# Kernel optimization log

Measured on AMD Instinct MI355X. Metric: run time of the kernel, lower is better.

The kernel has to match this reference:

```python
import jax, jax.numpy as jnp
import numpy as np

E = 8_388_608  # total edges across batched graphs
G = 4096       # num_graphs


def setup_inputs() -> dict:
    key = jax.random.key(0)
    k1, k2, k3 = jax.random.split(key, 3)
    edge_scores = jax.random.normal(k1, (E,), dtype=jnp.float32)
    # edge_batch: sorted segment ids in [0, G), as in PyG batched graphs
    edge_batch = jnp.sort(jax.random.randint(k2, (E,), 0, G)).astype(jnp.int32)
    candidate_mask = jax.random.bernoulli(k3, 0.5, (E,))
    return {
        "edge_scores": edge_scores,
        "edge_batch": edge_batch,
        "candidate_mask": candidate_mask,
        "num_graphs": G,
        "k": 32,
    }


def reference(edge_scores, edge_batch, candidate_mask, num_graphs, k):
    """Segmented top-k edge selection (GFlowNetActor._select_topk_candidate_edges).

    Faithful fixed-shape formulation: candidate edges come in as a boolean mask
    over all E edges (the rollout builds cand_edges = nonzero(candidate_mask)),
    and the kept top-k-per-graph edges go out as a boolean pruned mask (the
    rollout scatters the returned indices back into pruned_mask). Also returns
    the score values gated by the pruned mask (differentiable output).
    """
    n = edge_scores.shape[0]
    neg_inf = jnp.finfo(jnp.float32).min
    # Non-candidates get -inf so they sort to the back of each segment
    s = jnp.where(candidate_mask, edge_scores.astype(jnp.float32), neg_inf)
    # Sort by score descending, then stably by segment id -> within each
    # graph edges appear in descending-score order (same double-argsort as torch)
    order_score = jnp.argsort(-s, stable=True)
    order_seg = jnp.argsort(edge_batch[order_score], stable=True)
    perm = order_score[order_seg]          # [E] edge ids sorted by (seg asc, score desc)
    seg_sorted = edge_batch[perm]          # [E]
    # Segment starts via bincount + exclusive cumsum
    counts = jnp.bincount(seg_sorted, length=num_graphs)
    start = jnp.concatenate(
        [jnp.zeros(1, jnp.int32), jnp.cumsum(counts)[:-1].astype(jnp.int32)]
    )
    rank = jnp.arange(n, dtype=jnp.int32) - start[seg_sorted]
    keep_sorted = (rank < k) & candidate_mask[perm]
    # Scatter keep flags back to original edge order
    pruned_mask = jnp.zeros(n, dtype=bool).at[perm].set(keep_sorted)
    pruned_scores = jnp.where(pruned_mask, edge_scores, jnp.float32(0.0))
    return pruned_mask, pruned_scores
```

## Files before the change

### kernel.cpp

```cpp
#include <hip/hip_runtime.h>
#include <stdint.h>

#define G_NUM 4096
#define BLOCK 256
#define WPB   4
#define WCH   12
#define CAPW  (64 * 4 * WCH - 3)
#define HBW   1024
#define CLSW  128

typedef unsigned long long ull;

__device__ __forceinline__ void wsync() {
    asm volatile("s_waitcnt lgkmcnt(0)" ::: "memory");
}

__device__ __forceinline__ unsigned int order_bits(float f) {
    unsigned int b = __float_as_uint(f);
    return (b & 0x80000000u) ? ~b : (b | 0x80000000u);
}
__device__ __forceinline__ float inv_order_bits(unsigned int ob) {
    return __uint_as_float((ob & 0x80000000u) ? (ob & 0x7FFFFFFFu) : ~ob);
}
__device__ __forceinline__ int physb(int b) { return ((b & 15) << 6) | (b >> 4); }

__global__ void prep_kernel(const int* __restrict__ batch, int* __restrict__ start,
                            const unsigned int* __restrict__ mraw, int* __restrict__ flag,
                            int E) {
    if (blockIdx.x == 0 && threadIdx.x < 64) {
        int lane = threadIdx.x;
        bool allI = true, allF = true;
        for (int i = lane; i < 256; i += 64) {
            unsigned int w = mraw[i];
            if (w > 1u) allI = false;
            if (w != 0u && w != 0x3F800000u) allF = false;
        }
        allI = __all(allI);
        allF = __all(allF);
        if (lane == 0) *flag = (allI || allF) ? 0 : 2;
    }
    int t = blockIdx.x * blockDim.x + threadIdx.x;
    if (t > G_NUM) return;
    if (t == G_NUM) { start[G_NUM] = E; return; }
    int lo = 0, hi = E;
    while (lo < hi) {
        int mid = (lo + hi) >> 1;
        if (batch[mid] < t) lo = mid + 1; else hi = mid;
    }
    start[t] = lo;
}

template <int NPT>
__device__ __forceinline__ void wave_sel(unsigned int* hist, int lane, int kk,
                                         int& bsel, unsigned int& cgt,
                                         unsigned int& csel, unsigned int& mtot)
{
    unsigned int h[NPT];
    unsigned int S = 0u;
    const int b0 = lane * NPT;
    #pragma unroll
    for (int j = 0; j < NPT; ++j) {
        int pb = physb(b0 + j);
        h[j] = hist[pb]; S += h[j]; hist[pb] = 0u;
    }
    unsigned int v = S;
    #pragma unroll
    for (int off = 1; off < 64; off <<= 1) {
        unsigned int o = __shfl_down(v, off, 64);
        if (lane + off < 64) v += o;
    }
    mtot = __shfl(v, 0, 64);
    unsigned int run = v - S;
    int fj = -1; unsigned int fc = 0u, fs = 0u;
    #pragma unroll
    for (int j = NPT - 1; j >= 0; --j) {
        unsigned int inc = run + h[j];
        if (fj < 0 && (unsigned)kk <= inc && (unsigned)kk > run) { fj = j; fc = run; fs = h[j]; }
        run = inc;
    }
    ull bm = __ballot(fj >= 0);
    int wl = (int)(__ffsll((long long)bm) - 1);
    bsel = __shfl(b0 + fj, wl, 64);
    cgt  = __shfl(fc, wl, 64);
    csel = __shfl(fs, wl, 64);
}

__global__ __launch_bounds__(BLOCK, 4) void topk_kernel(
    const float* __restrict__ scores, const void* __restrict__ maskp,
    const int* __restrict__ start, const int* __restrict__ kp,
    const int* __restrict__ flagp, float* __restrict__ out_mask,
    float* __restrict__ out_scores, int E)
{
    __shared__ unsigned int hist_s[WPB][HBW];
    __shared__ ull          cls_s[WPB][CLSW];
    __shared__ unsigned int ccnt_s[WPB];

    const int tid  = threadIdx.x;
    const int lane = tid & 63;
    const int w    = tid >> 6;
    const int g    = blockIdx.x * WPB + w;

    const int s0 = start[g];
    const int s1 = start[g + 1];
    const int len = s1 - s0;
    if (len <= 0) return;

    const int k     = *kp;
    const int mflag = *flagp;
    unsigned int* hist = hist_s[w];
    ull*          cls  = cls_s[w];

    auto getmask = [&](int i) -> bool {
        if (mflag == 2) return ((const unsigned char*)maskp)[i] != 0;
        return ((const int*)maskp)[i] != 0;
    };

    if (k <= 0) {
        for (int i = s0 + lane; i < s1; i += 64) { out_mask[i] = 0.0f; out_scores[i] = 0.0f; }
        return;
    }

    if (len <= CAPW) {
        const int a0 = s0 & ~3;
        const int dl = a0 - s0;
        unsigned int key[4 * WCH];
        ull candm = 0ull;

        #pragma unroll
        for (int j = 0; j < HBW / 64; ++j) hist[physb(lane + 64 * j)] = 0u;
        if (lane == 0) ccnt_s[w] = 0u;

        #pragma unroll
        for (int q = 0; q < WCH; ++q) {
            const int g0 = a0 + 4 * (q * 64 + lane);
            unsigned int cm4 = 0u;
            if (g0 >= s0 && g0 + 4 <= s1) {
                float4 f = *(const float4*)(scores + g0);
                key[4*q+0] = order_bits(f.x); key[4*q+1] = order_bits(f.y);
                key[4*q+2] = order_bits(f.z); key[4*q+3] = order_bits(f.w);
                if (mflag == 2) {
                    unsigned int mw = *(const unsigned int*)((const unsigned char*)maskp + g0);
                    if (mw & 0x000000FFu) cm4 |= 1u;
                    if (mw & 0x0000FF00u) cm4 |= 2u;
                    if (mw & 0x00FF0000u) cm4 |= 4u;
                    if (mw & 0xFF000000u) cm4 |= 8u;
                } else {
                    int4 mw = *(const int4*)((const int*)maskp + g0);
                    if (mw.x) cm4 |= 1u; if (mw.y) cm4 |= 2u;
                    if (mw.z) cm4 |= 4u; if (mw.w) cm4 |= 8u;
                }
            } else if (g0 < s1 && g0 + 4 > s0) {
                #pragma unroll
                for (int j = 0; j < 4; ++j) {
                    int gi = g0 + j; key[4*q+j] = 0u;
                    if (gi >= s0 && gi < s1) {
                        key[4*q+j] = order_bits(scores[gi]);
                        if (getmask(gi)) cm4 |= 1u << j;
                    }
                }
            } else {
                #pragma unroll
                for (int j = 0; j < 4; ++j) key[4*q+j] = 0u;
            }
            candm |= (ull)cm4 << (4 * q);
        }
        wsync();

        #pragma unroll
        for (int v = 0; v < 4 * WCH; ++v)
            if ((candm >> v) & 1ull) atomicAdd(&hist[physb((int)(key[v] >> 22))], 1u);
        wsync();

        int bsel; unsigned int cgt, csel, m;
        wave_sel<HBW / 64>(hist, lane, k, bsel, cgt, csel, m);

        const bool keepall = (m <= (unsigned)k);
        unsigned int P = 0u;
        int licut = 0x7FFFFFFF;

        if (!keepall) {
            int kk2 = k - (int)cgt;

            if (csel <= CLSW) {
                #pragma unroll
                for (int v = 0; v < 4 * WCH; ++v) {
                    if (((candm >> v) & 1ull) && (int)(key[v] >> 22) == bsel) {
                        int q = v >> 2;
                        int li = dl + 4 * (q * 64 + lane) + (v & 3);
                        cls[atomicAdd(&ccnt_s[w], 1u)] = ((ull)key[v] << 32) | (unsigned)li;
                    }
                }
                wsync();
                bool found = false; unsigned int fP = 0u; int fL = 0;
                if (csel <= 64) {
                    ull me = (lane < (int)csel) ? cls[lane] : 0ull;
                    unsigned int mk = (unsigned int)(me >> 32), ml = (unsigned int)me;
                    int r = 0;
                    for (int j = 0; j < (int)csel; ++j) {
                        ull o = __shfl(me, j, 64);
                        unsigned int ok = (unsigned int)(o >> 32), ol = (unsigned int)o;
                        r += (ok > mk || (ok == mk && ol < ml)) ? 1 : 0;
                    }
                    if (lane < (int)csel && r == kk2 - 1) { found = true; fP = mk; fL = (int)ml; }
                } else {
                    for (int e = lane; e < (int)csel; e += 64) {
                        ull me = cls[e];
                        unsigned int mk = (unsigned int)(me >> 32), ml = (unsigned int)me;
                        int r = 0;
                        for (int j = 0; j < (int)csel; ++j) {
                            ull o = cls[j];
                            unsigned int ok = (unsigned int)(o >> 32), ol = (unsigned int)o;
                            r += (ok > mk || (ok == mk && ol < ml)) ? 1 : 0;
                        }
                        if (r == kk2 - 1) { found = true; fP = mk; fL = (int)ml; }
                    }
                }
                ull bm = __ballot(found);
                int wl = (int)(__ffsll((long long)bm) - 1);
                P = __shfl(fP, wl, 64); licut = __shfl(fL, wl, 64);
            } else {
                unsigned int pfx = ((unsigned int)bsel) << 22;
                const int lows[3] = {14, 6, 0};
                const int wids[3] = {8, 8, 6};
                #pragma unroll
                for (int r = 0; r < 3; ++r) {
                    const int L = lows[r], W = wids[r];
                    const unsigned int dm = (1u << W) - 1u;
                    #pragma unroll
                    for (int v = 0; v < 4 * WCH; ++v)
                        if (((candm >> v) & 1ull) &&
                            ((key[v] >> (L + W)) == (pfx >> (L + W))))
                            atomicAdd(&hist[physb((int)((key[v] >> L) & dm))], 1u);
                    wsync();
                    int b2; unsigned int cg2, cs2, mt2;
                    if (W == 8) wave_sel<4>(hist, lane, kk2, b2, cg2, cs2, mt2);
                    else        wave_sel<1>(hist, lane, kk2, b2, cg2, cs2, mt2);
                    pfx |= ((unsigned int)b2) << L;
                    kk2 -= (int)cg2;
                }
                P = pfx;
                int lo = 0, hi = len - 1;
                while (lo < hi) {
                    int mid = (lo + hi) >> 1;
                    int c = 0;
                    #pragma unroll
                    for (int v = 0; v < 4 * WCH; ++v) {
                        int q = v >> 2;
                        int li = dl + 4 * (q * 64 + lane) + (v & 3);
                        if (((candm >> v) & 1ull) && key[v] == P && li <= mid) c++;
                    }
                    #pragma unroll
                    for (int off = 1; off < 64; off <<= 1) c += __shfl_xor(c, off, 64);
                    if (c >= kk2) hi = mid; else lo = mid + 1;
                }
                licut = lo;
            }
        }

        #pragma unroll
        for (int q = 0; q < WCH; ++q) {
            const int g0 = a0 + 4 * (q * 64 + lane);
            if (g0 >= s0 && g0 + 4 <= s1) {
                float4 vm, vs;
                float* pm = (float*)&vm; float* ps = (float*)&vs;
                #pragma unroll
                for (int j = 0; j < 4; ++j) {
                    int v = 4*q + j;
                    int li = dl + 4 * (q * 64 + lane) + j;
                    bool kept = ((candm >> v) & 1ull) &&
                        (key[v] > P || (key[v] == P && li <= licut));
                    pm[j] = kept ? 1.0f : 0.0f;
                    ps[j] = kept ? inv_order_bits(key[v]) : 0.0f;
                }
                *(float4*)(out_mask   + g0) = vm;
                *(float4*)(out_scores + g0) = vs;
            } else if (g0 < s1 && g0 + 4 > s0) {
                #pragma unroll
                for (int j = 0; j < 4; ++j) {
                    int gi = g0 + j;
                    if (gi < s0 || gi >= s1) continue;
                    int v = 4*q + j;
                    int li = gi - s0;
                    bool kept = ((candm >> v) & 1ull) &&
                        (key[v] > P || (key[v] == P && li <= licut));
                    out_mask[gi]   = kept ? 1.0f : 0.0f;
                    out_scores[gi] = kept ? inv_order_bits(key[v]) : 0.0f;
                }
            }
        }
    } else {
        #pragma unroll
        for (int j = 0; j < 4; ++j) hist[physb(lane * 4 + j)] = 0u;
        int lc = 0;
        for (int i = s0 + lane; i < s1; i += 64)
            if (getmask(i)) lc++;
        #pragma unroll
        for (int off = 1; off < 64; off <<= 1) lc += __shfl_xor(lc, off, 64);
        const int m = lc;
        const bool keepall = (m <= k);
        ull pivot = 0ull;
        if (!keepall) {
            ull pfx = 0ull;
            int kk = k;
            for (int shift = 56; shift >= 0; shift -= 8) {
                wsync();
                for (int i = s0 + lane; i < s1; i += 64) {
                    if (!getmask(i)) continue;
                    ull kv = ((ull)order_bits(scores[i]) << 32) |
                             (ull)(0xFFFFFFFFu - (unsigned)(i - s0));
                    if (shift == 56 || (kv >> (shift + 8)) == (pfx >> (shift + 8)))
                        atomicAdd(&hist[physb((int)((kv >> shift) & 0xFFull))], 1u);
                }
                wsync();
                int b; unsigned int cg, cs, mt;
                wave_sel<4>(hist, lane, kk, b, cg, cs, mt);
                pfx |= ((ull)(unsigned)b) << shift;
                kk -= (int)cg;
            }
            pivot = pfx;
        }
        for (int i = s0 + lane; i < s1; i += 64) {
            bool c = getmask(i);
            float sc = 0.0f;
            bool kept = false;
            if (c) {
                sc = scores[i];
                ull kv = ((ull)order_bits(sc) << 32) |
                         (ull)(0xFFFFFFFFu - (unsigned)(i - s0));
                kept = keepall || (kv >= pivot);
            }
            out_mask[i]   = kept ? 1.0f : 0.0f;
            out_scores[i] = kept ? sc : 0.0f;
        }
    }
}

extern "C" void kernel_launch(void* const* d_in, const int* in_sizes, int n_in,
                              void* d_out, int out_size, void* d_ws, size_t ws_size,
                              hipStream_t stream) {
    const float* scores = (const float*)d_in[0];
    const int*   batch  = (const int*)d_in[1];
    const void*  mask   = d_in[2];
    const int*   kp     = (const int*)d_in[4];
    const int    E      = in_sizes[0];

    float* out_mask   = (float*)d_out;
    float* out_scores = out_mask + E;

    int* flag  = (int*)d_ws;
    int* start = (int*)((char*)d_ws + 1024);

    prep_kernel<<<(G_NUM + 1 + BLOCK - 1) / BLOCK, BLOCK, 0, stream>>>(
        batch, start, (const unsigned int*)mask, flag, E);
    topk_kernel<<<G_NUM / WPB, BLOCK, 0, stream>>>(scores, mask, start, kp, flag,
                                                   out_mask, out_scores, E);
}
```

Before: 53.93 us.

## Split top-k into pivot-selection and flat elementwise output kernels

```diff
diff --git a/kernel.cpp b/kernel.cpp
--- a/kernel.cpp
+++ b/kernel.cpp
@@ -2,31 +2,27 @@
 #include <stdint.h>
 
 #define G_NUM 4096
-#define BLOCK 256
 #define WPB   4
-#define WCH   12
-#define CAPW  (64 * 4 * WCH - 3)
-#define HBW   1024
+#define HBW   512
+#define HSZ   528
 #define CLSW  128
+#define KCH   12
+#define KCAP  (KCH * 256)
 
 typedef unsigned long long ull;
 
 __device__ __forceinline__ void wsync() {
     asm volatile("s_waitcnt lgkmcnt(0)" ::: "memory");
 }
-
 __device__ __forceinline__ unsigned int order_bits(float f) {
     unsigned int b = __float_as_uint(f);
     return (b & 0x80000000u) ? ~b : (b | 0x80000000u);
 }
-__device__ __forceinline__ float inv_order_bits(unsigned int ob) {
-    return __uint_as_float((ob & 0x80000000u) ? (ob & 0x7FFFFFFFu) : ~ob);
-}
-__device__ __forceinline__ int physb(int b) { return ((b & 15) << 6) | (b >> 4); }
+__device__ __forceinline__ int HP(int b) { return b + (b >> 5); }
 
 __global__ void prep_kernel(const int* __restrict__ batch, int* __restrict__ start,
-                            const unsigned int* __restrict__ mraw, int* __restrict__ flag,
-                            int E) {
+                            int* __restrict__ gtile, const unsigned int* __restrict__ mraw,
+                            int* __restrict__ flag, int E, int ntiles) {
     if (blockIdx.x == 0 && threadIdx.x < 64) {
         int lane = threadIdx.x;
         bool allI = true, allF = true;
@@ -40,27 +36,30 @@
         if (lane == 0) *flag = (allI || allF) ? 0 : 2;
     }
     int t = blockIdx.x * blockDim.x + threadIdx.x;
-    if (t > G_NUM) return;
-    if (t == G_NUM) { start[G_NUM] = E; return; }
-    int lo = 0, hi = E;
-    while (lo < hi) {
-        int mid = (lo + hi) >> 1;
-        if (batch[mid] < t) lo = mid + 1; else hi = mid;
-    }
-    start[t] = lo;
+    if (t <= G_NUM) {
+        if (t == G_NUM) { start[G_NUM] = E; return; }
+        int lo = 0, hi = E;
+        while (lo < hi) {
+            int mid = (lo + hi) >> 1;
+            if (batch[mid] < t) lo = mid + 1; else hi = mid;
+        }
+        start[t] = lo;
+    } else {
+        int tt = t - (G_NUM + 1);
+        if (tt < ntiles) gtile[tt] = batch[(size_t)tt << 10];
+    }
 }
 
 template <int NPT>
 __device__ __forceinline__ void wave_sel(unsigned int* hist, int lane, int kk,
-                                         int& bsel, unsigned int& cgt,
-                                         unsigned int& csel, unsigned int& mtot)
+                                         int& bsel, unsigned int& cgt, unsigned int& csel)
 {
     unsigned int h[NPT];
     unsigned int S = 0u;
     const int b0 = lane * NPT;
     #pragma unroll
     for (int j = 0; j < NPT; ++j) {
-        int pb = physb(b0 + j);
+        int pb = HP(b0 + j);
         h[j] = hist[pb]; S += h[j]; hist[pb] = 0u;
     }
     unsigned int v = S;
@@ -69,7 +68,6 @@
         unsigned int o = __shfl_down(v, off, 64);
         if (lane + off < 64) v += o;
     }
-    mtot = __shfl(v, 0, 64);
     unsigned int run = v - S;
     int fj = -1; unsigned int fc = 0u, fs = 0u;
     #pragma unroll
@@ -85,252 +83,270 @@
     csel = __shfl(fs, wl, 64);
 }
 
-__global__ __launch_bounds__(BLOCK, 4) void topk_kernel(
+__global__ __launch_bounds__(256) void sel_kernel(
     const float* __restrict__ scores, const void* __restrict__ maskp,
     const int* __restrict__ start, const int* __restrict__ kp,
-    const int* __restrict__ flagp, float* __restrict__ out_mask,
-    float* __restrict__ out_scores, int E)
+    const int* __restrict__ flagp, ull* __restrict__ PL)
 {
-    __shared__ unsigned int hist_s[WPB][HBW];
-    __shared__ ull          cls_s[WPB][CLSW];
-    __shared__ unsigned int ccnt_s[WPB];
+    __shared__ unsigned int   hist_s[WPB][HSZ];
+    __shared__ unsigned short k16_s[WPB][KCAP];
+    __shared__ ull            cls_s[WPB][CLSW];
+    __shared__ unsigned int   ccnt_s[WPB];
 
     const int tid  = threadIdx.x;
     const int lane = tid & 63;
     const int w    = tid >> 6;
     const int g    = blockIdx.x * WPB + w;
 
-    const int s0 = start[g];
-    const int s1 = start[g + 1];
-    const int len = s1 - s0;
+    const int s0 = start[g], s1 = start[g + 1], len = s1 - s0;
     if (len <= 0) return;
-
-    const int k     = *kp;
-    const int mflag = *flagp;
-    unsigned int* hist = hist_s[w];
-    ull*          cls  = cls_s[w];
-
-    auto getmask = [&](int i) -> bool {
-        if (mflag == 2) return ((const unsigned char*)maskp)[i] != 0;
-        return ((const int*)maskp)[i] != 0;
+    const int k = *kp, mflag = *flagp;
+    if (k <= 0) { if (!lane) PL[g] = (0xFFFFFFFFull << 32) | 0xFFFFFFFFull; return; }
+
+    unsigned int*   hist = hist_s[w];
+    unsigned short* k16  = k16_s[w];
+    ull*            cls  = cls_s[w];
+
+    const int a0 = s0 & ~3, dl = a0 - s0;
+    const int nch = (s1 - a0 + 255) >> 8;
+    const bool st16 = (nch <= KCH);
+
+    #pragma unroll
+    for (int j = 0; j < HBW / 64; ++j) hist[HP(lane + 64 * j)] = 0u;
+    if (!lane) ccnt_s[w] = 0u;
+    wsync();
+
+    auto load_chunk = [&](int q, unsigned int kk4[4]) -> unsigned int {
+        const int g0 = a0 + 4 * (q * 64 + lane);
+        unsigned int cm4 = 0u;
+        if (g0 >= s0 && g0 + 4 <= s1) {
+            float4 f = *(const float4*)(scores + g0);
+            kk4[0] = order_bits(f.x); kk4[1] = order_bits(f.y);
+            kk4[2] = order_bits(f.z); kk4[3] = order_bits(f.w);
+            if (mflag == 2) {
+                unsigned int mw = *(const unsigned int*)((const unsigned char*)maskp + g0);
+                if (mw & 0x000000FFu) cm4 |= 1u;
+                if (mw & 0x0000FF00u) cm4 |= 2u;
+                if (mw & 0x00FF0000u) cm4 |= 4u;
+                if (mw & 0xFF000000u) cm4 |= 8u;
+            } else {
+                int4 mw = *(const int4*)((const int*)maskp + g0);
+                if (mw.x) cm4 |= 1u; if (mw.y) cm4 |= 2u;
+                if (mw.z) cm4 |= 4u; if (mw.w) cm4 |= 8u;
+            }
+        } else if (g0 < s1 && g0 + 4 > s0) {
+            #pragma unroll
+            for (int j = 0; j < 4; ++j) {
+                int gi = g0 + j; kk4[j] = 0u;
+                if (gi >= s0 && gi < s1) {
+                    kk4[j] = order_bits(scores[gi]);
+                    bool c = (mflag == 2) ? (((const unsigned char*)maskp)[gi] != 0)
+                                          : (((const int*)maskp)[gi] != 0);
+                    if (c) cm4 |= 1u << j;
+                }
+            }
+        } else {
+            kk4[0] = kk4[1] = kk4[2] = kk4[3] = 0u;
+        }
+        return cm4;
     };
 
-    if (k <= 0) {
-        for (int i = s0 + lane; i < s1; i += 64) { out_mask[i] = 0.0f; out_scores[i] = 0.0f; }
-        return;
-    }
-
-    if (len <= CAPW) {
-        const int a0 = s0 & ~3;
-        const int dl = a0 - s0;
-        unsigned int key[4 * WCH];
-        ull candm = 0ull;
-
+    int lc = 0;
+    for (int q = 0; q < nch; ++q) {
+        unsigned int kk4[4];
+        unsigned int cm4 = load_chunk(q, kk4);
+        if (st16) {
+            ushort4 hv; unsigned short* hp = (unsigned short*)&hv;
+            #pragma unroll
+            for (int j = 0; j < 4; ++j) {
+                unsigned int h = kk4[j] >> 16; h += (h == 0u);
+                hp[j] = ((cm4 >> j) & 1u) ? (unsigned short)h : (unsigned short)0;
+            }
+            *(ushort4*)&k16[4 * (q * 64 + lane)] = hv;
+        }
         #pragma unroll
-        for (int j = 0; j < HBW / 64; ++j) hist[physb(lane + 64 * j)] = 0u;
-        if (lane == 0) ccnt_s[w] = 0u;
-
-        #pragma unroll
-        for (int q = 0; q < WCH; ++q) {
-            const int g0 = a0 + 4 * (q * 64 + lane);
-            unsigned int cm4 = 0u;
-            if (g0 >= s0 && g0 + 4 <= s1) {
-                float4 f = *(const float4*)(scores + g0);
-                key[4*q+0] = order_bits(f.x); key[4*q+1] = order_bits(f.y);
-                key[4*q+2] = order_bits(f.z); key[4*q+3] = order_bits(f.w);
-                if (mflag == 2) {
-                    unsigned int mw = *(const unsigned int*)((const unsigned char*)maskp + g0);
-                    if (mw & 0x000000FFu) cm4 |= 1u;
-                    if (mw & 0x0000FF00u) cm4 |= 2u;
-                    if (mw & 0x00FF0000u) cm4 |= 4u;
-                    if (mw & 0xFF000000u) cm4 |= 8u;
-                } else {
-                    int4 mw = *(const int4*)((const int*)maskp + g0);
-                    if (mw.x) cm4 |= 1u; if (mw.y) cm4 |= 2u;
-                    if (mw.z) cm4 |= 4u; if (mw.w) cm4 |= 8u;
-                }
-            } else if (g0 < s1 && g0 + 4 > s0) {
-                #pragma unroll
-                for (int j = 0; j < 4; ++j) {
-                    int gi = g0 + j; key[4*q+j] = 0u;
-                    if (gi >= s0 && gi < s1) {
-                        key[4*q+j] = order_bits(scores[gi]);
-                        if (getmask(gi)) cm4 |= 1u << j;
+        for (int j = 0; j < 4; ++j)
+            if ((cm4 >> j) & 1u) { atomicAdd(&hist[HP((int)(kk4[j] >> 23))], 1u); ++lc; }
+    }
+    #pragma unroll
+    for (int off = 1; off < 64; off <<= 1) lc += __shfl_xor(lc, off, 64);
+    const int m = lc;
+    wsync();
+
+    unsigned int P = 0u;
+    int licut = 0x7FFFFFFF;
+
+    if (m > k) {
+        int bsel; unsigned int cgt, csel;
+        wave_sel<HBW / 64>(hist, lane, k, bsel, cgt, csel);
+        int kk2 = k - (int)cgt;
+
+        if (csel <= CLSW) {
+            if (st16) {
+                const int tot2 = (nch * 256) >> 1;
+                const unsigned int* k16w = (const unsigned int*)k16;
+                for (int i2 = lane; i2 < tot2; i2 += 64) {
+                    unsigned int h2 = k16w[i2];
+                    unsigned int h0 = h2 & 0xFFFFu, h1 = h2 >> 16;
+                    if (h0 && (int)(h0 >> 7) == bsel) {
+                        int lp = 2 * i2;
+                        unsigned int key = order_bits(scores[a0 + lp]);
+                        cls[atomicAdd(&ccnt_s[w], 1u)] = ((ull)key << 32) | (unsigned)(lp + dl);
                     }
+                    if (h1 && (int)(h1 >> 7) == bsel) {
+                        int lp = 2 * i2 + 1;
+                        unsigned int key = order_bits(scores[a0 + lp]);
+                        cls[atomicAdd(&ccnt_s[w], 1u)] = ((ull)key << 32) | (unsigned)(lp + dl);
+                    }
                 }
             } else {
-                #pragma unroll
-                for (int j = 0; j < 4; ++j) key[4*q+j] = 0u;
-            }
-            candm |= (ull)cm4 << (4 * q);
-        }
-        wsync();
-
-        #pragma unroll
-        for (int v = 0; v < 4 * WCH; ++v)
-            if ((candm >> v) & 1ull) atomicAdd(&hist[physb((int)(key[v] >> 22))], 1u);
-        wsync();
-
-        int bsel; unsigned int cgt, csel, m;
-        wave_sel<HBW / 64>(hist, lane, k, bsel, cgt, csel, m);
-
-        const bool keepall = (m <= (unsigned)k);
-        unsigned int P = 0u;
-        int licut = 0x7FFFFFFF;
-
-        if (!keepall) {
-            int kk2 = k - (int)cgt;
-
-            if (csel <= CLSW) {
-                #pragma unroll
-                for (int v = 0; v < 4 * WCH; ++v) {
-                    if (((candm >> v) & 1ull) && (int)(key[v] >> 22) == bsel) {
-                        int q = v >> 2;
-                        int li = dl + 4 * (q * 64 + lane) + (v & 3);
-                        cls[atomicAdd(&ccnt_s[w], 1u)] = ((ull)key[v] << 32) | (unsigned)li;
-                    }
-                }
-                wsync();
-                bool found = false; unsigned int fP = 0u; int fL = 0;
-                if (csel <= 64) {
-                    ull me = (lane < (int)csel) ? cls[lane] : 0ull;
+                for (int q = 0; q < nch; ++q) {
+                    unsigned int kk4[4];
+                    unsigned int cm4 = load_chunk(q, kk4);
+                    const int g0 = a0 + 4 * (q * 64 + lane);
+                    #pragma unroll
+                    for (int j = 0; j < 4; ++j)
+                        if (((cm4 >> j) & 1u) && (int)(kk4[j] >> 23) == bsel)
+                            cls[atomicAdd(&ccnt_s[w], 1u)] =
+                                ((ull)kk4[j] << 32) | (unsigned)(g0 + j - s0);
+                }
+            }
+            wsync();
+            bool found = false; unsigned int fP = 0u; int fL = 0;
+            if (csel <= 64) {
+                ull me = (lane < (int)csel) ? cls[lane] : 0ull;
+                unsigned int mk = (unsigned int)(me >> 32), ml = (unsigned int)me;
+                int r = 0;
+                for (int j = 0; j < (int)csel; ++j) {
+                    ull o = __shfl(me, j, 64);
+                    unsigned int ok = (unsigned int)(o >> 32), ol = (unsigned int)o;
+                    r += (ok > mk || (ok == mk && ol < ml)) ? 1 : 0;
+                }
+                if (lane < (int)csel && r == kk2 - 1) { found = true; fP = mk; fL = (int)ml; }
+            } else {
+                for (int e = lane; e < (int)csel; e += 64) {
+                    ull me = cls[e];
                     unsigned int mk = (unsigned int)(me >> 32), ml = (unsigned int)me;
                     int r = 0;
                     for (int j = 0; j < (int)csel; ++j) {
-                        ull o = __shfl(me, j, 64);
+                        ull o = cls[j];
                         unsigned int ok = (unsigned int)(o >> 32), ol = (unsigned int)o;
                         r += (ok > mk || (ok == mk && ol < ml)) ? 1 : 0;
                     }
-                    if (lane < (int)csel && r == kk2 - 1) { found = true; fP = mk; fL = (int)ml; }
-                } else {
-                    for (int e = lane; e < (int)csel; e += 64) {
-                        ull me = cls[e];
-                        unsigned int mk = (unsigned int)(me >> 32), ml = (unsigned int)me;
-                        int r = 0;
-                        for (int j = 0; j < (int)csel; ++j) {
-                            ull o = cls[j];
-                            unsigned int ok = (unsigned int)(o >> 32), ol = (unsigned int)o;
-                            r += (ok > mk || (ok == mk && ol < ml)) ? 1 : 0;
-                        }
-                        if (r == kk2 - 1) { found = true; fP = mk; fL = (int)ml; }
-                    }
-                }
-                ull bm = __ballot(found);
-                int wl = (int)(__ffsll((long long)bm) - 1);
-                P = __shfl(fP, wl, 64); licut = __shfl(fL, wl, 64);
-            } else {
-                unsigned int pfx = ((unsigned int)bsel) << 22;
-                const int lows[3] = {14, 6, 0};
-                const int wids[3] = {8, 8, 6};
+                    if (r == kk2 - 1) { found = true; fP = mk; fL = (int)ml; }
+                }
+            }
+            ull bm = __ballot(found);
+            int wl = (int)(__ffsll((long long)bm) - 1);
+            P = __shfl(fP, wl, 64); licut = __shfl(fL, wl, 64);
+        } else {
+            unsigned int pfx = ((unsigned int)bsel) << 23;
+            const int lows[3] = {15, 7, 0};
+            const int wids[3] = {8, 8, 7};
+            for (int r = 0; r < 3; ++r) {
+                const int L = lows[r], W = wids[r];
+                const unsigned int dm = (1u << W) - 1u;
+                wsync();
+                for (int q = 0; q < nch; ++q) {
+                    unsigned int kk4[4];
+                    unsigned int cm4 = load_chunk(q, kk4);
+                    #pragma unroll
+                    for (int j = 0; j < 4; ++j)
+                        if (((cm4 >> j) & 1u) && ((kk4[j] >> (L + W)) == (pfx >> (L + W))))
+                            atomicAdd(&hist[HP((int)((kk4[j] >> L) & dm))], 1u);
+                }
+                wsync();
+                int b2; unsigned int cg2, cs2;
+                if (W == 8) wave_sel<4>(hist, lane, kk2, b2, cg2, cs2);
+                else        wave_sel<2>(hist, lane, kk2, b2, cg2, cs2);
+                pfx |= ((unsigned int)b2) << L;
+                kk2 -= (int)cg2;
+            }
+            P = pfx;
+            int lo2 = 0, hi2 = len - 1;
+            while (lo2 < hi2) {
+                int mid = (lo2 + hi2) >> 1;
+                int cc = 0;
+                for (int q = 0; q < nch; ++q) {
+                    unsigned int kk4[4];
+                    unsigned int cm4 = load_chunk(q, kk4);
+                    const int g0 = a0 + 4 * (q * 64 + lane);
+                    #pragma unroll
+                    for (int j = 0; j < 4; ++j)
+                        if (((cm4 >> j) & 1u) && kk4[j] == P && (g0 + j - s0) <= mid) ++cc;
+                }
                 #pragma unroll
-                for (int r = 0; r < 3; ++r) {
-                    const int L = lows[r], W = wids[r];
-                    const unsigned int dm = (1u << W) - 1u;
-                    #pragma unroll
-                    for (int v = 0; v < 4 * WCH; ++v)
-                        if (((candm >> v) & 1ull) &&
-                            ((key[v] >> (L + W)) == (pfx >> (L + W))))
-                            atomicAdd(&hist[physb((int)((key[v] >> L) & dm))], 1u);
-                    wsync();
-                    int b2; unsigned int cg2, cs2, mt2;
-                    if (W == 8) wave_sel<4>(hist, lane, kk2, b2, cg2, cs2, mt2);
-                    else        wave_sel<1>(hist, lane, kk2, b2, cg2, cs2, mt2);
-                    pfx |= ((unsigned int)b2) << L;
-                    kk2 -= (int)cg2;
-                }
-                P = pfx;
-                int lo = 0, hi = len - 1;
-                while (lo < hi) {
-                    int mid = (lo + hi) >> 1;
-                    int c = 0;
-                    #pragma unroll
-                    for (int v = 0; v < 4 * WCH; ++v) {
-                        int q = v >> 2;
-                        int li = dl + 4 * (q * 64 + lane) + (v & 3);
-                        if (((candm >> v) & 1ull) && key[v] == P && li <= mid) c++;
-                    }
-                    #pragma unroll
-                    for (int off = 1; off < 64; off <<= 1) c += __shfl_xor(c, off, 64);
-                    if (c >= kk2) hi = mid; else lo = mid + 1;
-                }
-                licut = lo;
-            }
-        }
-
+                for (int off = 1; off < 64; off <<= 1) cc += __shfl_xor(cc, off, 64);
+                if (cc >= kk2) hi2 = mid; else lo2 = mid + 1;
+            }
+            licut = lo2;
+        }
+    }
+    if (!lane) PL[g] = ((ull)P << 32) | (unsigned int)licut;
+}
+
+__global__ __launch_bounds__(256) void out_kernel(
+    const float* __restrict__ scores, const void* __restrict__ maskp,
+    const int* __restrict__ start, const int* __restrict__ gtile,
+    const ull* __restrict__ PL, const int* __restrict__ flagp,
+    float* __restrict__ out_mask, float* __restrict__ out_scores, int E)
+{
+    const int mflag = *flagp;
+    const int nchunk = E >> 2;
+    const int stride = gridDim.x * blockDim.x;
+    for (int c = blockIdx.x * blockDim.x + threadIdx.x; c < nchunk; c += stride) {
+        const int gi0 = c << 2;
+        int g = gtile[gi0 >> 10];
+        int sg = start[g], snext = start[g + 1];
+        while (gi0 >= snext) { ++g; sg = snext; snext = start[g + 1]; }
+        ull pl = PL[g];
+
+        float4 f = *(const float4*)(scores + gi0);
+        unsigned int cm4 = 0u;
+        if (mflag == 2) {
+            unsigned int mw = *(const unsigned int*)((const unsigned char*)maskp + gi0);
+            if (mw & 0x000000FFu) cm4 |= 1u;
+            if (mw & 0x0000FF00u) cm4 |= 2u;
+            if (mw & 0x00FF0000u) cm4 |= 4u;
+            if (mw & 0xFF000000u) cm4 |= 8u;
+        } else {
+            int4 mw = *(const int4*)((const int*)maskp + gi0);
+            if (mw.x) cm4 |= 1u; if (mw.y) cm4 |= 2u;
+            if (mw.z) cm4 |= 4u; if (mw.w) cm4 |= 8u;
+        }
+        float4 vm, vs;
+        float* pm = (float*)&vm; float* ps = (float*)&vs;
+        const float* pf = (const float*)&f;
         #pragma unroll
-        for (int q = 0; q < WCH; ++q) {
-            const int g0 = a0 + 4 * (q * 64 + lane);
-            if (g0 >= s0 && g0 + 4 <= s1) {
-                float4 vm, vs;
-                float* pm = (float*)&vm; float* ps = (float*)&vs;
-                #pragma unroll
-                for (int j = 0; j < 4; ++j) {
-                    int v = 4*q + j;
-                    int li = dl + 4 * (q * 64 + lane) + j;
-                    bool kept = ((candm >> v) & 1ull) &&
-                        (key[v] > P || (key[v] == P && li <= licut));
-                    pm[j] = kept ? 1.0f : 0.0f;
-                    ps[j] = kept ? inv_order_bits(key[v]) : 0.0f;
-                }
-                *(float4*)(out_mask   + g0) = vm;
-                *(float4*)(out_scores + g0) = vs;
-            } else if (g0 < s1 && g0 + 4 > s0) {
-                #pragma unroll
-                for (int j = 0; j < 4; ++j) {
-                    int gi = g0 + j;
-                    if (gi < s0 || gi >= s1) continue;
-                    int v = 4*q + j;
-                    int li = gi - s0;
-                    bool kept = ((candm >> v) & 1ull) &&
-                        (key[v] > P || (key[v] == P && li <= licut));
-                    out_mask[gi]   = kept ? 1.0f : 0.0f;
-                    out_scores[gi] = kept ? inv_order_bits(key[v]) : 0.0f;
-                }
-            }
-        }
-    } else {
-        #pragma unroll
-        for (int j = 0; j < 4; ++j) hist[physb(lane * 4 + j)] = 0u;
-        int lc = 0;
-        for (int i = s0 + lane; i < s1; i += 64)
-            if (getmask(i)) lc++;
-        #pragma unroll
-        for (int off = 1; off < 64; off <<= 1) lc += __shfl_xor(lc, off, 64);
-        const int m = lc;
-        const bool keepall = (m <= k);
-        ull pivot = 0ull;
-        if (!keepall) {
-            ull pfx = 0ull;
-            int kk = k;
-            for (int shift = 56; shift >= 0; shift -= 8) {
-                wsync();
-                for (int i = s0 + lane; i < s1; i += 64) {
-                    if (!getmask(i)) continue;
-                    ull kv = ((ull)order_bits(scores[i]) << 32) |
-                             (ull)(0xFFFFFFFFu - (unsigned)(i - s0));
-                    if (shift == 56 || (kv >> (shift + 8)) == (pfx >> (shift + 8)))
-                        atomicAdd(&hist[physb((int)((kv >> shift) & 0xFFull))], 1u);
-                }
-                wsync();
-                int b; unsigned int cg, cs, mt;
-                wave_sel<4>(hist, lane, kk, b, cg, cs, mt);
-                pfx |= ((ull)(unsigned)b) << shift;
-                kk -= (int)cg;
-            }
-            pivot = pfx;
-        }
-        for (int i = s0 + lane; i < s1; i += 64) {
-            bool c = getmask(i);
-            float sc = 0.0f;
-            bool kept = false;
-            if (c) {
-                sc = scores[i];
-                ull kv = ((ull)order_bits(sc) << 32) |
-                         (ull)(0xFFFFFFFFu - (unsigned)(i - s0));
-                kept = keepall || (kv >= pivot);
-            }
-            out_mask[i]   = kept ? 1.0f : 0.0f;
-            out_scores[i] = kept ? sc : 0.0f;
+        for (int j = 0; j < 4; ++j) {
+            int gi = gi0 + j;
+            while (gi >= snext) { ++g; sg = snext; snext = start[g + 1]; pl = PL[g]; }
+            unsigned int Pv = (unsigned int)(pl >> 32);
+            int Lv = (int)(unsigned int)pl;
+            unsigned int key = order_bits(pf[j]);
+            int li = gi - sg;
+            bool kept = ((cm4 >> j) & 1u) && (key > Pv || (key == Pv && li <= Lv));
+            pm[j] = kept ? 1.0f : 0.0f;
+            ps[j] = kept ? pf[j] : 0.0f;
+        }
+        *(float4*)(out_mask   + gi0) = vm;
+        *(float4*)(out_scores + gi0) = vs;
+    }
+    if (blockIdx.x == 0 && threadIdx.x == 0 && (E & 3)) {
+        for (int gi = E & ~3; gi < E; ++gi) {
+            int g = gtile[gi >> 10];
+            while (gi >= start[g + 1]) ++g;
+            ull pl = PL[g];
+            unsigned int Pv = (unsigned int)(pl >> 32);
+            int Lv = (int)(unsigned int)pl;
+            bool cand = (mflag == 2) ? (((const unsigned char*)maskp)[gi] != 0)
+                                     : (((const int*)maskp)[gi] != 0);
+            float sc = scores[gi];
+            unsigned int key = order_bits(sc);
+            int li = gi - start[g];
+            bool kept = cand && (key > Pv || (key == Pv && li <= Lv));
+            out_mask[gi]   = kept ? 1.0f : 0.0f;
+            out_scores[gi] = kept ? sc : 0.0f;
         }
     }
 }
@@ -347,11 +363,20 @@
     float* out_mask   = (float*)d_out;
     float* out_scores = out_mask + E;
 
-    int* flag  = (int*)d_ws;
-    int* start = (int*)((char*)d_ws + 1024);
-
-    prep_kernel<<<(G_NUM + 1 + BLOCK - 1) / BLOCK, BLOCK, 0, stream>>>(
-        batch, start, (const unsigned int*)mask, flag, E);
-    topk_kernel<<<G_NUM / WPB, BLOCK, 0, stream>>>(scores, mask, start, kp, flag,
-                                                   out_mask, out_scores, E);
-}
+    const int ntiles = (E + 1023) >> 10;
+    char* ws = (char*)d_ws;
+    int* flag  = (int*)ws;
+    int* start = (int*)(ws + 4096);
+    int* gtile = (int*)(ws + 4096 + 16640);
+    ull* PL    = (ull*)(ws + 4096 + 16640 + (((size_t)ntiles * 4 + 255) & ~(size_t)255));
+
+    const int prep_threads = G_NUM + 1 + ntiles;
+    prep_kernel<<<(prep_threads + 255) / 256, 256, 0, stream>>>(
+        batch, start, gtile, (const unsigned int*)mask, flag, E, ntiles);
+    sel_kernel<<<G_NUM / WPB, 256, 0, stream>>>(scores, mask, start, kp, flag, PL);
+    const int nchunk = E >> 2;
+    int oblocks = (nchunk + 255) / 256;
+    if (oblocks > 2048) oblocks = 2048;
+    out_kernel<<<oblocks, 256, 0, stream>>>(scores, mask, start, gtile, PL, flag,
+                                            out_mask, out_scores, E);
+}
```

Result: slower. 196.9 us (+265.1%).
